# Optimization experiments

Hardware: AMD Instinct MI355X
Metric: run time of the kernel (lower is better)

## Reference

```python
import jax, jax.numpy as jnp
import numpy as np

H = 12       # num attention heads
D = 64       # head dim
K = 6        # heads activated: max(1, int(H * top_k_percent)), top_k_percent=0.5
EPS = 1e-12  # BERT LayerNorm eps


def setup_inputs() -> dict:
    key = jax.random.key(0)
    ks = jax.random.split(key, 8)
    hid = H * D
    sc = 0.02
    return {
        'hidden_states': jax.random.normal(ks[0], (8, 1024, hid), jnp.float32),
        'Wq': jax.random.normal(ks[1], (hid, hid), jnp.float32) * sc,
        'bq': jnp.zeros((hid,), jnp.float32),
        'Wk': jax.random.normal(ks[2], (hid, hid), jnp.float32) * sc,
        'bk': jnp.zeros((hid,), jnp.float32),
        'Wv': jax.random.normal(ks[3], (hid, hid), jnp.float32) * sc,
        'bv': jnp.zeros((hid,), jnp.float32),
        'Wr': jax.random.normal(ks[4], (hid, H), jnp.float32) * sc,
        'br': jnp.zeros((H,), jnp.float32),
        'Wo': jax.random.normal(ks[5], (hid, hid), jnp.float32) * sc,
        'bo': jnp.zeros((hid,), jnp.float32),
        'ln_g': jnp.ones((hid,), jnp.float32),
        'ln_b': jnp.zeros((hid,), jnp.float32),
    }


def reference(hidden_states, Wq, bq, Wk, bk, Wv, bv, Wr, br, Wo, bo, ln_g, ln_b):
    B, S, hid = hidden_states.shape
    # Router: mean-pooled tokens -> per-head logits -> straight-through top-k mask
    router_in = hidden_states.mean(axis=1)                      # [B, hid]
    logits = router_in @ Wr + br                                # [B, H]
    _, top_idx = jax.lax.top_k(logits, K)                       # [B, K]
    hard = jax.nn.one_hot(top_idx, H, dtype=logits.dtype).sum(axis=1)  # [B, H]
    head_mask = hard + logits - jax.lax.stop_gradient(logits)   # straight-through
    m = head_mask[:, :, None, None]                             # [B, H, 1, 1]

    def proj(W, b):
        return (hidden_states @ W + b).reshape(B, S, H, D).transpose(0, 2, 1, 3)

    q = proj(Wq, bq) * m
    k = proj(Wk, bk) * m
    v = proj(Wv, bv) * m

    scores = jnp.einsum('bhqd,bhkd->bhqk', q, k) / jnp.sqrt(jnp.float32(D))
    probs = jax.nn.softmax(scores, axis=-1)
    ctx = jnp.einsum('bhqk,bhkd->bhqd', probs, v)               # [B, H, S, D]
    ctx = ctx.transpose(0, 2, 1, 3).reshape(B, S, hid)

    # BertSelfOutput: dense -> (dropout=identity in eval) -> residual -> LayerNorm
    x = ctx @ Wo + bo + hidden_states
    mu = x.mean(axis=-1, keepdims=True)
    var = ((x - mu) ** 2).mean(axis=-1, keepdims=True)
    return ((x - mu) / jnp.sqrt(var + EPS)) * ln_g + ln_b
```

## Files before the change

kernel.cpp:

```cpp
#include <hip/hip_runtime.h>

typedef __bf16 bf16;
typedef __bf16 bf16x2_t __attribute__((ext_vector_type(2)));
typedef __bf16 bf16x4_t __attribute__((ext_vector_type(4)));
typedef __bf16 bf16x8 __attribute__((ext_vector_type(8)));
typedef float  f32x4  __attribute__((ext_vector_type(4)));

__device__ __forceinline__ void async16(const void* g, void* l) {
  __builtin_amdgcn_global_load_lds(
      (__attribute__((address_space(1))) void*)(g),
      (__attribute__((address_space(3))) void*)(l), 16, 0, 0);
}

__device__ __forceinline__ f32x4 mfma16(bf16x8 a, bf16x8 b, f32x4 c) {
  return __builtin_amdgcn_mfma_f32_16x16x32_bf16(a, b, c, 0, 0, 0);
}

__global__ __launch_bounds__(256) void prep_k(
    const float* __restrict__ hs, bf16* __restrict__ hsb, float* __restrict__ partial,
    const float* __restrict__ s0, const float* __restrict__ s1,
    const float* __restrict__ s2, const float* __restrict__ s3,
    bf16* __restrict__ d0, bf16* __restrict__ d1,
    bf16* __restrict__ d2, bf16* __restrict__ d3) {
  __shared__ bf16 tile[32][33];
  int id = blockIdx.x;
  int t = threadIdx.x;
  if (id < 2304) {
    int z = id / 576, rem = id % 576;
    int by = rem / 24, bx = rem % 24;
    const float* in = (z == 0) ? s0 : (z == 1) ? s1 : (z == 2) ? s2 : s3;
    bf16* out       = (z == 0) ? d0 : (z == 1) ? d1 : (z == 2) ? d2 : d3;
    int c0 = bx * 32, r0 = by * 32;
#pragma unroll
    for (int i = 0; i < 4; ++i) {
      int idx = t + i * 256;
      int r = idx >> 5, c = idx & 31;
      tile[r][c] = (bf16)in[(size_t)(r0 + r) * 768 + (c0 + c)];
    }
    __syncthreads();
#pragma unroll
    for (int i = 0; i < 4; ++i) {
      int idx = t + i * 256;
      int r = idx >> 5, c = idx & 31;
      out[(size_t)(c0 + r) * 768 + (r0 + c)] = tile[c][r];
    }
  } else {
    int id2 = id - 2304;
    int b = id2 & 7, g = id2 >> 3;
    if (t >= 192) return;
    const float* p = hs  + ((size_t)b * 1024 + g * 32) * 768 + t * 4;
    bf16*        q = hsb + ((size_t)b * 1024 + g * 32) * 768 + t * 4;
    float4 a = {0.f, 0.f, 0.f, 0.f};
    for (int s = 0; s < 32; ++s) {
      float4 v = *(const float4*)(p + (size_t)s * 768);
      a.x += v.x; a.y += v.y; a.z += v.z; a.w += v.w;
      bf16x4_t o;
      o[0] = (bf16)v.x; o[1] = (bf16)v.y; o[2] = (bf16)v.z; o[3] = (bf16)v.w;
      *(bf16x4_t*)(q + (size_t)s * 768) = o;
    }
    *(float4*)(partial + ((size_t)b * 32 + g) * 768 + t * 4) = a;
  }
}

__global__ __launch_bounds__(256) void router_final_k(const float* __restrict__ Wr,
                                                      const float* __restrict__ br,
                                                      const float* __restrict__ partial,
                                                      float* __restrict__ mask,
                                                      int* __restrict__ actH) {
  int b = blockIdx.x, t = threadIdx.x;
  int w = t >> 6;
  __shared__ float mean_s[768];
  __shared__ float red[4][12];
  __shared__ float lg[12];
  for (int c = t; c < 768; c += 256) {
    float a = 0.f;
    for (int g = 0; g < 32; ++g) a += partial[((size_t)b * 32 + g) * 768 + c];
    mean_s[c] = a * (1.0f / 1024.0f);
  }
  __syncthreads();
  float a[12];
#pragma unroll
  for (int h = 0; h < 12; ++h) a[h] = 0.f;
#pragma unroll
  for (int j = 0; j < 3; ++j) {
    int c = t + j * 256;
    float m = mean_s[c];
    const float* wr = Wr + c * 12;
#pragma unroll
    for (int h = 0; h < 12; ++h) a[h] += m * wr[h];
  }
#pragma unroll
  for (int off = 1; off < 64; off <<= 1)
#pragma unroll
    for (int h = 0; h < 12; ++h) a[h] += __shfl_xor(a[h], off);
  if ((t & 63) == 0)
#pragma unroll
    for (int h = 0; h < 12; ++h) red[w][h] = a[h];
  __syncthreads();
  if (t == 0) {
#pragma unroll
    for (int h = 0; h < 12; ++h)
      lg[h] = br[h] + red[0][h] + red[1][h] + red[2][h] + red[3][h];
    unsigned chosen = 0;
    for (int j = 0; j < 6; ++j) {
      int bi = -1; float bv = -1e30f;
      for (int h = 0; h < 12; ++h)
        if (!((chosen >> h) & 1) && lg[h] > bv) { bv = lg[h]; bi = h; }
      chosen |= 1u << bi;
    }
    int k = 0;
    for (int h = 0; h < 12; ++h) {
      mask[b * 12 + h] = ((chosen >> h) & 1) ? 1.f : 0.f;
      if ((chosen >> h) & 1) actH[b * 6 + (k++)] = h;
    }
  }
}

__global__ __launch_bounds__(256, 3) void gemm_qkv_k(
    const bf16* __restrict__ X, const bf16* __restrict__ Wcat,
    const float* __restrict__ bq, const float* __restrict__ bk, const float* __restrict__ bv,
    const int* __restrict__ actH,
    bf16* __restrict__ Qo, bf16* __restrict__ Ko, bf16* __restrict__ Vto) {
  __shared__ __align__(16) bf16 Al[128 * 64];
  __shared__ __align__(16) bf16 Bl[128 * 64];
  int mt64 = blockIdx.x;
  int sp   = blockIdx.y;
  int z    = blockIdx.z;
  int b    = mt64 >> 3;
  int h0   = actH[b * 6 + sp * 2];
  int h1   = actH[b * 6 + sp * 2 + 1];
  int m0   = mt64 * 128;

  const float* bia = (z == 0) ? bq : (z == 1) ? bk : bv;
  int t = threadIdx.x, w = t >> 6, lane = t & 63, lrow = lane & 15, quad = lane >> 4;
  int wm = (w >> 1) * 64, wn = (w & 1) * 64;

  int srow = t >> 3;
  int sch  = (t & 7) ^ (srow & 7);
  const bf16* aptr[4];
  const bf16* bptr[4];
#pragma unroll
  for (int i = 0; i < 4; ++i) {
    aptr[i] = X + (size_t)(m0 + i * 32 + srow) * 768 + sch * 8;
    int hh = (i < 2) ? h0 : h1;
    int rr = (i & 1) * 32 + srow;
    bptr[i] = Wcat + (size_t)(z * 768 + hh * 64 + rr) * 768 + sch * 8;
  }

  int ra_base = wm + lrow, rb_base = wn + lrow;
  const bf16* baA[2];
  const bf16* baB[2];
#pragma unroll
  for (int ks = 0; ks < 2; ++ks) {
    baA[ks] = &Al[ra_base * 64 + (((ks * 4 + quad) ^ (ra_base & 7)) * 8)];
    baB[ks] = &Bl[rb_base * 64 + (((ks * 4 + quad) ^ (rb_base & 7)) * 8)];
  }

  f32x4 acc[4][4];
#pragma unroll
  for (int a = 0; a < 4; ++a)
#pragma unroll
    for (int c = 0; c < 4; ++c) acc[a][c] = (f32x4){0.f, 0.f, 0.f, 0.f};

  for (int k0 = 0; k0 < 768; k0 += 64) {
#pragma unroll
    for (int i = 0; i < 4; ++i) {
      async16(aptr[i], &Al[(i * 256 + t) * 8]);
      aptr[i] += 64;
    }
#pragma unroll
    for (int i = 0; i < 4; ++i) {
      async16(bptr[i], &Bl[(i * 256 + t) * 8]);
      bptr[i] += 64;
    }
    __syncthreads();
    bf16x8 af[2][4], bfr[2][4];
#pragma unroll
    for (int ks = 0; ks < 2; ++ks)
#pragma unroll
      for (int i = 0; i < 4; ++i) {
        af[ks][i]  = *(const bf16x8*)(baA[ks] + i * 1024);
        bfr[ks][i] = *(const bf16x8*)(baB[ks] + i * 1024);
      }
#pragma unroll
    for (int ks = 0; ks < 2; ++ks)
#pragma unroll
      for (int mt = 0; mt < 4; ++mt)
#pragma unroll
        for (int nt2 = 0; nt2 < 4; ++nt2)
          acc[mt][nt2] = mfma16(af[ks][mt], bfr[ks][nt2], acc[mt][nt2]);
    __syncthreads();
  }

  float biasv[4];
#pragma unroll
  for (int nt2 = 0; nt2 < 4; ++nt2) {
    int nl = wn + nt2 * 16 + lrow;
    int hh = (nl >> 6) ? h1 : h0;
    biasv[nt2] = bia[hh * 64 + (nl & 63)];
  }

  if (z == 2) {
#pragma unroll
    for (int mt = 0; mt < 4; ++mt)
#pragma unroll
      for (int nt2 = 0; nt2 < 4; ++nt2) {
        int s = (m0 + wm + mt * 16 + quad * 4) & 1023;
        int nl = wn + nt2 * 16 + lrow;
        int hh = (nl >> 6) ? h1 : h0;
        int d = nl & 63;
        bf16x4_t pk;
#pragma unroll
        for (int r = 0; r < 4; ++r) pk[r] = (bf16)(acc[mt][nt2][r] + biasv[nt2]);
        *(bf16x4_t*)&Vto[(((size_t)b * 12 + hh) * 64 + d) * 1024 + s] = pk;
      }
  } else {
    bf16* Out = (z == 0) ? Qo : Ko;
#pragma unroll
    for (int mt = 0; mt < 4; ++mt)
#pragma unroll
      for (int nt2 = 0; nt2 < 4; ++nt2)
#pragma unroll
        for (int r = 0; r < 4; ++r) {
          int s = (m0 + wm + mt * 16 + quad * 4 + r) & 1023;
          int nl = wn + nt2 * 16 + lrow;
          int hh = (nl >> 6) ? h1 : h0;
          int d = nl & 63;
          Out[(((size_t)b * 12 + hh) * 1024 + s) * 64 + d] =
              (bf16)(acc[mt][nt2][r] + biasv[nt2]);
        }
  }
}

__global__ __launch_bounds__(256, 3) void attn_k(
    const bf16* __restrict__ Q, const bf16* __restrict__ K, const bf16* __restrict__ Vt,
    const int* __restrict__ actH, bf16* __restrict__ ctx) {
  int ai = blockIdx.x, qt = blockIdx.y;
  int bb = ai / 6, slot = ai - bb * 6;
  int h = actH[bb * 6 + slot];
  int bh = bb * 12 + h;
  int t = threadIdx.x, w = t >> 6, lane = t & 63, lrow = lane & 15, quad = lane >> 4;

  __shared__ __align__(16) bf16 K_lds[128 * 64];
  __shared__ __align__(16) bf16 V_lds[64 * 128];
  __shared__ __align__(16) bf16 P_lds[4][16 * 136];

  const bf16* Qh = Q  + (size_t)bh * 65536;
  const bf16* Kh = K  + (size_t)bh * 65536;
  const bf16* Vh = Vt + (size_t)bh * 65536;

  bf16x8 qf[2][2];
#pragma unroll
  for (int mt = 0; mt < 2; ++mt)
#pragma unroll
    for (int ks = 0; ks < 2; ++ks)
      qf[mt][ks] = *(const bf16x8*)&Qh[(size_t)(qt * 128 + w * 32 + mt * 16 + lrow) * 64 + ks * 32 + quad * 8];

  f32x4 o_acc[2][4];
  float m_i[2][4], l_i[2][4];
#pragma unroll
  for (int mt = 0; mt < 2; ++mt) {
#pragma unroll
    for (int dt = 0; dt < 4; ++dt) o_acc[mt][dt] = (f32x4){0.f, 0.f, 0.f, 0.f};
#pragma unroll
    for (int r = 0; r < 4; ++r) { m_i[mt][r] = -INFINITY; l_i[mt][r] = 0.f; }
  }

  for (int kt = 0; kt < 8; ++kt) {
#pragma unroll
    for (int i = 0; i < 4; ++i) {
      int c = i * 256 + t;
      int r = c >> 3, ch = (c & 7) ^ (r & 7);
      async16(Kh + (size_t)kt * 8192 + r * 64 + ch * 8, &K_lds[c * 8]);
    }
#pragma unroll
    for (int i = 0; i < 4; ++i) {
      int c = i * 256 + t;
      int r = c >> 4, ch = (c & 15) ^ (r & 7);
      async16(Vh + (size_t)r * 1024 + kt * 128 + ch * 8, &V_lds[c * 8]);
    }
    __syncthreads();

#pragma unroll
    for (int mt = 0; mt < 2; ++mt) {
      f32x4 s_acc[8];
#pragma unroll
      for (int nt = 0; nt < 8; ++nt) s_acc[nt] = (f32x4){0.f, 0.f, 0.f, 0.f};
      __builtin_amdgcn_s_setprio(1);
#pragma unroll
      for (int nt = 0; nt < 8; ++nt) {
        int rb = nt * 16 + lrow;
#pragma unroll
        for (int ks = 0; ks < 2; ++ks) {
          bf16x8 kf = *(const bf16x8*)&K_lds[rb * 64 + (((ks * 4 + quad) ^ (rb & 7)) * 8)];
          s_acc[nt] = mfma16(qf[mt][ks], kf, s_acc[nt]);
        }
      }
      __builtin_amdgcn_s_setprio(0);
#pragma unroll
      for (int nt = 0; nt < 8; ++nt) s_acc[nt] = s_acc[nt] * 0.125f;

      float mx[4];
#pragma unroll
      for (int r = 0; r < 4; ++r) {
        float m = s_acc[0][r];
#pragma unroll
        for (int nt = 1; nt < 8; ++nt) m = fmaxf(m, s_acc[nt][r]);
        m = fmaxf(m, __shfl_xor(m, 1));
        m = fmaxf(m, __shfl_xor(m, 2));
        m = fmaxf(m, __shfl_xor(m, 4));
        m = fmaxf(m, __shfl_xor(m, 8));
        mx[r] = m;
      }
      bool grow = false;
#pragma unroll
      for (int r = 0; r < 4; ++r) grow = grow || (mx[r] > m_i[mt][r] + 8.f);
      if (__any(grow)) {
#pragma unroll
        for (int r = 0; r < 4; ++r) {
          float mold = m_i[mt][r];
          float mnew = fmaxf(mold, mx[r]);
          float alpha = __expf(mold - mnew);
          m_i[mt][r] = mnew;
          l_i[mt][r] *= alpha;
#pragma unroll
          for (int dt = 0; dt < 4; ++dt) o_acc[mt][dt][r] *= alpha;
        }
      }
#pragma unroll
      for (int r = 0; r < 4; ++r) {
        float mnew = m_i[mt][r];
        float rs = 0.f;
#pragma unroll
        for (int nt = 0; nt < 8; ++nt) {
          float pv = __expf(s_acc[nt][r] - mnew);
          rs += pv;
          P_lds[w][(quad * 4 + r) * 136 + nt * 16 + lrow] = (bf16)pv;
        }
        rs += __shfl_xor(rs, 1);
        rs += __shfl_xor(rs, 2);
        rs += __shfl_xor(rs, 4);
        rs += __shfl_xor(rs, 8);
        l_i[mt][r] += rs;
      }

      bf16x8 pf[4];
#pragma unroll
      for (int ks = 0; ks < 4; ++ks)
        pf[ks] = *(const bf16x8*)&P_lds[w][lrow * 136 + ks * 32 + quad * 8];
      __builtin_amdgcn_s_setprio(1);
#pragma unroll
      for (int dt = 0; dt < 4; ++dt) {
        int rv = dt * 16 + lrow;
#pragma unroll
        for (int ks = 0; ks < 4; ++ks) {
          bf16x8 vf = *(const bf16x8*)&V_lds[rv * 128 + (((ks * 4 + quad) ^ (rv & 7)) * 8)];
          o_acc[mt][dt] = mfma16(pf[ks], vf, o_acc[mt][dt]);
        }
      }
      __builtin_amdgcn_s_setprio(0);
    }
    __syncthreads();
  }

#pragma unroll
  for (int mt = 0; mt < 2; ++mt)
#pragma unroll
    for (int r = 0; r < 4; ++r) {
      float inv = 1.0f / l_i[mt][r];
      int s = qt * 128 + w * 32 + mt * 16 + quad * 4 + r;
#pragma unroll
      for (int dt = 0; dt < 4; ++dt) {
        int d = dt * 16 + lrow;
        ctx[((size_t)(bb * 1024 + s)) * 768 + h * 64 + d] = (bf16)(o_acc[mt][dt][r] * inv);
      }
    }
}

__global__ __launch_bounds__(256, 3) void gemm_out_k(
    const bf16* __restrict__ Cx, const bf16* __restrict__ Wot,
    const float* __restrict__ bo, const float* __restrict__ res,
    const float* __restrict__ mask,
    float* __restrict__ xo) {
  __shared__ __align__(16) bf16 Al[128 * 64];
  __shared__ __align__(16) bf16 Bl[128 * 64];
  int bid = blockIdx.x;
  int xcd = bid & 7, idx = bid >> 3;
  int nt = idx % 6, mt8 = idx / 6;
  int m0 = (mt8 * 8 + xcd) * 128;
  int n0 = nt * 128;
  int t = threadIdx.x, w = t >> 6, lane = t & 63, lrow = lane & 15, quad = lane >> 4;
  int wm = (w >> 1) * 64, wn = (w & 1) * 64;

  int bb = m0 >> 10;
  unsigned am = 0;
#pragma unroll
  for (int hh = 0; hh < 12; ++hh)
    am |= (mask[bb * 12 + hh] != 0.f) ? (1u << hh) : 0u;

  int srow = t >> 3;
  int sch  = (t & 7) ^ (srow & 7);
  const bf16* aptr[4];
  const bf16* bptr[4];
#pragma unroll
  for (int i = 0; i < 4; ++i) {
    aptr[i] = Cx  + (size_t)(m0 + i * 32 + srow) * 768 + sch * 8;
    bptr[i] = Wot + (size_t)(n0 + i * 32 + srow) * 768 + sch * 8;
  }
  int ra_base = wm + lrow, rb_base = wn + lrow;
  const bf16* baA[2];
  const bf16* baB[2];
#pragma unroll
  for (int ks = 0; ks < 2; ++ks) {
    baA[ks] = &Al[ra_base * 64 + (((ks * 4 + quad) ^ (ra_base & 7)) * 8)];
    baB[ks] = &Bl[rb_base * 64 + (((ks * 4 + quad) ^ (rb_base & 7)) * 8)];
  }

  f32x4 acc[4][4];
#pragma unroll
  for (int a = 0; a < 4; ++a)
#pragma unroll
    for (int b = 0; b < 4; ++b) acc[a][b] = (f32x4){0.f, 0.f, 0.f, 0.f};

  for (int k0 = 0; k0 < 768; k0 += 64) {
    if (am & (1u << (k0 >> 6))) {
#pragma unroll
      for (int i = 0; i < 4; ++i) async16(aptr[i], &Al[(i * 256 + t) * 8]);
#pragma unroll
      for (int i = 0; i < 4; ++i) async16(bptr[i], &Bl[(i * 256 + t) * 8]);
      __syncthreads();
      bf16x8 af[2][4], bfr[2][4];
#pragma unroll
      for (int ks = 0; ks < 2; ++ks)
#pragma unroll
        for (int i = 0; i < 4; ++i) {
          af[ks][i]  = *(const bf16x8*)(baA[ks] + i * 1024);
          bfr[ks][i] = *(const bf16x8*)(baB[ks] + i * 1024);
        }
#pragma unroll
      for (int ks = 0; ks < 2; ++ks)
#pragma unroll
        for (int mt = 0; mt < 4; ++mt)
#pragma unroll
          for (int nt2 = 0; nt2 < 4; ++nt2)
            acc[mt][nt2] = mfma16(af[ks][mt], bfr[ks][nt2], acc[mt][nt2]);
      __syncthreads();
    }
#pragma unroll
    for (int i = 0; i < 4; ++i) { aptr[i] += 64; bptr[i] += 64; }
  }

  float biasv[4];
#pragma unroll
  for (int nt2 = 0; nt2 < 4; ++nt2) biasv[nt2] = bo[n0 + wn + nt2 * 16 + lrow];

#pragma unroll
  for (int mt = 0; mt < 4; ++mt)
#pragma unroll
    for (int nt2 = 0; nt2 < 4; ++nt2)
#pragma unroll
      for (int r = 0; r < 4; ++r) {
        int m = m0 + wm + mt * 16 + quad * 4 + r;
        int n = n0 + wn + nt2 * 16 + lrow;
        xo[(size_t)m * 768 + n] = acc[mt][nt2][r] + biasv[nt2] + res[(size_t)m * 768 + n];
      }
}

__global__ __launch_bounds__(256) void ln_k(const float* __restrict__ x,
                                            const float* __restrict__ g,
                                            const float* __restrict__ be,
                                            float* __restrict__ out) {
  int t = threadIdx.x, w = t >> 6, lane = t & 63;
  int row = blockIdx.x * 4 + w;
  const float4* xr4 = (const float4*)(x + (size_t)row * 768);
  float4 v0 = xr4[lane], v1 = xr4[lane + 64], v2 = xr4[lane + 128];
  float s  = v0.x + v0.y + v0.z + v0.w + v1.x + v1.y + v1.z + v1.w
           + v2.x + v2.y + v2.z + v2.w;
  float s2 = v0.x*v0.x + v0.y*v0.y + v0.z*v0.z + v0.w*v0.w
           + v1.x*v1.x + v1.y*v1.y + v1.z*v1.z + v1.w*v1.w
           + v2.x*v2.x + v2.y*v2.y + v2.z*v2.z + v2.w*v2.w;
#pragma unroll
  for (int off = 32; off > 0; off >>= 1) {
    s  += __shfl_xor(s, off);
    s2 += __shfl_xor(s2, off);
  }
  float mu = s * (1.0f / 768.0f);
  float var = s2 * (1.0f / 768.0f) - mu * mu;
  float rsq = rsqrtf(var + 1e-12f);
  const float4* g4 = (const float4*)g;
  const float4* b4 = (const float4*)be;
  float4* or4 = (float4*)(out + (size_t)row * 768);
  float4 gv, bv, o;
  gv = g4[lane];       bv = b4[lane];
  o.x = (v0.x - mu) * rsq * gv.x + bv.x; o.y = (v0.y - mu) * rsq * gv.y + bv.y;
  o.z = (v0.z - mu) * rsq * gv.z + bv.z; o.w = (v0.w - mu) * rsq * gv.w + bv.w;
  or4[lane] = o;
  gv = g4[lane + 64];  bv = b4[lane + 64];
  o.x = (v1.x - mu) * rsq * gv.x + bv.x; o.y = (v1.y - mu) * rsq * gv.y + bv.y;
  o.z = (v1.z - mu) * rsq * gv.z + bv.z; o.w = (v1.w - mu) * rsq * gv.w + bv.w;
  or4[lane + 64] = o;
  gv = g4[lane + 128]; bv = b4[lane + 128];
  o.x = (v2.x - mu) * rsq * gv.x + bv.x; o.y = (v2.y - mu) * rsq * gv.y + bv.y;
  o.z = (v2.z - mu) * rsq * gv.z + bv.z; o.w = (v2.w - mu) * rsq * gv.w + bv.w;
  or4[lane + 128] = o;
}

extern "C" void kernel_launch(void* const* d_in, const int* in_sizes, int n_in,
                              void* d_out, int out_size, void* d_ws, size_t ws_size,
                              hipStream_t stream) {
  const float* hs  = (const float*)d_in[0];
  const float* Wq  = (const float*)d_in[1];
  const float* bq  = (const float*)d_in[2];
  const float* Wk  = (const float*)d_in[3];
  const float* bk  = (const float*)d_in[4];
  const float* Wv  = (const float*)d_in[5];
  const float* bv  = (const float*)d_in[6];
  const float* Wr  = (const float*)d_in[7];
  const float* br  = (const float*)d_in[8];
  const float* Wo  = (const float*)d_in[9];
  const float* bo  = (const float*)d_in[10];
  const float* lng = (const float*)d_in[11];
  const float* lnb = (const float*)d_in[12];
  float* out = (float*)d_out;
  dim3 blk(256);

  char* p = (char*)d_ws;
  float* maskp = (float*)p; p += 512;
  int*   actI  = (int*)p;   p += 256;
  float* partial = (float*)p; p += (size_t)8 * 32 * 768 * 4;
  bf16* hsb  = (bf16*)p; p += (size_t)8192 * 768 * 2;
  bf16* Wcat = (bf16*)p; p += (size_t)2304 * 768 * 2;
  bf16* Wot  = (bf16*)p; p += (size_t)768 * 768 * 2;

  prep_k<<<dim3(2560), blk, 0, stream>>>(hs, hsb, partial,
      Wq, Wk, Wv, Wo, Wcat, Wcat + 768 * 768, Wcat + 1536 * 768, Wot);
  router_final_k<<<dim3(8), blk, 0, stream>>>(Wr, br, partial, maskp, actI);

  size_t used_common = (size_t)(p - (char*)d_ws);
  size_t need_big = used_common + 3 * (size_t)8192 * 768 * 2;

  if (ws_size >= need_big) {
    char* qk_base = p;
    bf16* Qb  = (bf16*)p; p += (size_t)8192 * 768 * 2;
    bf16* Kb  = (bf16*)p; p += (size_t)8192 * 768 * 2;
    bf16* Vtb = (bf16*)p;
    float* Xb = (float*)qk_base;
    bf16* Ctx = (bf16*)d_out;

    gemm_qkv_k<<<dim3(64, 3, 3), blk, 0, stream>>>(hsb, Wcat, bq, bk, bv, actI, Qb, Kb, Vtb);
    attn_k<<<dim3(48, 8), blk, 0, stream>>>(Qb, Kb, Vtb, actI, Ctx);
    gemm_out_k<<<dim3(8 * 8 * 6), blk, 0, stream>>>(Ctx, Wot, bo, hs, maskp, Xb);
    ln_k<<<dim3(2048), blk, 0, stream>>>(Xb, lng, lnb, out);
  } else {
    bf16* Qb  = (bf16*)p; p += (size_t)1024 * 768 * 2;
    bf16* Kb  = (bf16*)p; p += (size_t)1024 * 768 * 2;
    bf16* Vtb = (bf16*)p; p += (size_t)1024 * 768 * 2;
    bf16* Ctx = (bf16*)p; p += (size_t)1024 * 768 * 2;
    float* Xb = (float*)p; p += (size_t)1024 * 768 * 4;

    for (int b = 0; b < 8; ++b) {
      const bf16* hsb_b = hsb + (size_t)b * 1024 * 768;
      const float* hs_b = hs + (size_t)b * 1024 * 768;
      float* outb = out + (size_t)b * 1024 * 768;
      gemm_qkv_k<<<dim3(8, 3, 3), blk, 0, stream>>>(hsb_b, Wcat, bq, bk, bv, actI + b * 6, Qb, Kb, Vtb);
      attn_k<<<dim3(6, 8), blk, 0, stream>>>(Qb, Kb, Vtb, actI + b * 6, Ctx);
      gemm_out_k<<<dim3(8 * 1 * 6), blk, 0, stream>>>(Ctx, Wot, bo, hs_b, maskp + b * 12, Xb);
      ln_k<<<dim3(256), blk, 0, stream>>>(Xb, lng, lnb, outb);
    }
  }
}
```

Before: 210.8 us.

## Split attention over two key halves with a flash-decoding style combine kernel

The attention kernel now splits the 1024-key sequence into two halves along a new grid z dimension, doubling the block count from 384 to 768 so the GPU's compute units are better filled. Each half writes unnormalised bf16 partial outputs plus per-row max and sum, and a new combine kernel merges them with log-sum-exp rescaling into the context buffer. This adds an extra launch, a round trip of partial results through memory, and bf16 rounding of the unnormalised partials. The context buffer is also moved into the hsb region.

```diff
diff --git a/kernel.cpp b/kernel.cpp
--- a/kernel.cpp
+++ b/kernel.cpp
@@ -234,8 +234,10 @@
 
 __global__ __launch_bounds__(256, 3) void attn_k(
     const bf16* __restrict__ Q, const bf16* __restrict__ K, const bf16* __restrict__ Vt,
-    const int* __restrict__ actH, bf16* __restrict__ ctx) {
-  int ai = blockIdx.x, qt = blockIdx.y;
+    const int* __restrict__ actH,
+    bf16* __restrict__ opart, float* __restrict__ mpart, float* __restrict__ lpart,
+    int nbh) {
+  int ai = blockIdx.x, qt = blockIdx.y, z = blockIdx.z;
   int bb = ai / 6, slot = ai - bb * 6;
   int h = actH[bb * 6 + slot];
   int bh = bb * 12 + h;
@@ -246,8 +248,9 @@
   __shared__ __align__(16) bf16 P_lds[4][16 * 136];
 
   const bf16* Qh = Q  + (size_t)bh * 65536;
-  const bf16* Kh = K  + (size_t)bh * 65536;
+  const bf16* Kh = K  + (size_t)bh * 65536 + (size_t)z * 32768;
   const bf16* Vh = Vt + (size_t)bh * 65536;
+  int vcol0 = z * 512;
 
   bf16x8 qf[2][2];
 #pragma unroll
@@ -266,7 +269,7 @@
     for (int r = 0; r < 4; ++r) { m_i[mt][r] = -INFINITY; l_i[mt][r] = 0.f; }
   }
 
-  for (int kt = 0; kt < 8; ++kt) {
+  for (int kt = 0; kt < 4; ++kt) {
 #pragma unroll
     for (int i = 0; i < 4; ++i) {
       int c = i * 256 + t;
@@ -277,7 +280,7 @@
     for (int i = 0; i < 4; ++i) {
       int c = i * 256 + t;
       int r = c >> 4, ch = (c & 15) ^ (r & 7);
-      async16(Vh + (size_t)r * 1024 + kt * 128 + ch * 8, &V_lds[c * 8]);
+      async16(Vh + (size_t)r * 1024 + vcol0 + kt * 128 + ch * 8, &V_lds[c * 8]);
     }
     __syncthreads();
 
@@ -363,18 +366,45 @@
     __syncthreads();
   }
 
+  size_t tile = ((size_t)(z * nbh + ai) * 8 + qt);
 #pragma unroll
   for (int mt = 0; mt < 2; ++mt)
 #pragma unroll
     for (int r = 0; r < 4; ++r) {
-      float inv = 1.0f / l_i[mt][r];
-      int s = qt * 128 + w * 32 + mt * 16 + quad * 4 + r;
-#pragma unroll
-      for (int dt = 0; dt < 4; ++dt) {
-        int d = dt * 16 + lrow;
-        ctx[((size_t)(bb * 1024 + s)) * 768 + h * 64 + d] = (bf16)(o_acc[mt][dt][r] * inv);
-      }
-    }
+      int srow = w * 32 + mt * 16 + quad * 4 + r;
+      if (lrow == 0) {
+        mpart[tile * 128 + srow] = m_i[mt][r];
+        lpart[tile * 128 + srow] = l_i[mt][r];
+      }
+#pragma unroll
+      for (int dt = 0; dt < 4; ++dt)
+        opart[(tile * 128 + srow) * 64 + dt * 16 + lrow] = (bf16)o_acc[mt][dt][r];
+    }
+}
+
+__global__ __launch_bounds__(256) void combine_k(
+    const bf16* __restrict__ opart, const float* __restrict__ mpart,
+    const float* __restrict__ lpart, const int* __restrict__ actH,
+    bf16* __restrict__ ctx, int nbh) {
+  int ai = blockIdx.x, qt = blockIdx.y;
+  int bb = ai / 6, slot = ai - bb * 6;
+  int h = actH[bb * 6 + slot];
+  int t = threadIdx.x, w = t >> 6, lane = t & 63;
+  size_t t1 = ((size_t)ai * 8 + qt) * 128;
+  size_t t2 = ((size_t)(nbh + ai) * 8 + qt) * 128;
+  for (int i = 0; i < 32; ++i) {
+    int row = w * 32 + i;
+    float m1 = mpart[t1 + row], l1 = lpart[t1 + row];
+    float m2 = mpart[t2 + row], l2 = lpart[t2 + row];
+    float M = fmaxf(m1, m2);
+    float a1 = __expf(m1 - M), a2 = __expf(m2 - M);
+    float inv = 1.0f / (l1 * a1 + l2 * a2);
+    float o1 = (float)opart[(t1 + row) * 64 + lane];
+    float o2 = (float)opart[(t2 + row) * 64 + lane];
+    int s = qt * 128 + row;
+    ctx[((size_t)(bb * 1024 + s)) * 768 + h * 64 + lane] =
+        (bf16)((o1 * a1 + o2 * a2) * inv);
+  }
 }
 
 __global__ __launch_bounds__(256, 3) void gemm_out_k(
@@ -545,10 +575,14 @@
     bf16* Kb  = (bf16*)p; p += (size_t)8192 * 768 * 2;
     bf16* Vtb = (bf16*)p;
     float* Xb = (float*)qk_base;
-    bf16* Ctx = (bf16*)d_out;
+    bf16* Ctx = hsb;
+    bf16*  opart = (bf16*)d_out;
+    float* mpart = (float*)((char*)d_out + (size_t)13 * 1024 * 1024);
+    float* lpart = mpart + 2 * 48 * 8 * 128;
 
     gemm_qkv_k<<<dim3(64, 3, 3), blk, 0, stream>>>(hsb, Wcat, bq, bk, bv, actI, Qb, Kb, Vtb);
-    attn_k<<<dim3(48, 8), blk, 0, stream>>>(Qb, Kb, Vtb, actI, Ctx);
+    attn_k<<<dim3(48, 8, 2), blk, 0, stream>>>(Qb, Kb, Vtb, actI, opart, mpart, lpart, 48);
+    combine_k<<<dim3(48, 8), blk, 0, stream>>>(opart, mpart, lpart, actI, Ctx, 48);
     gemm_out_k<<<dim3(8 * 8 * 6), blk, 0, stream>>>(Ctx, Wot, bo, hs, maskp, Xb);
     ln_k<<<dim3(2048), blk, 0, stream>>>(Xb, lng, lnb, out);
   } else {
@@ -557,13 +591,17 @@
     bf16* Vtb = (bf16*)p; p += (size_t)1024 * 768 * 2;
     bf16* Ctx = (bf16*)p; p += (size_t)1024 * 768 * 2;
     float* Xb = (float*)p; p += (size_t)1024 * 768 * 4;
+    bf16*  opart = (bf16*)p; p += (size_t)2 * 6 * 8 * 128 * 64 * 2;
+    float* mpart = (float*)p; p += (size_t)2 * 6 * 8 * 128 * 4;
+    float* lpart = (float*)p; p += (size_t)2 * 6 * 8 * 128 * 4;
 
     for (int b = 0; b < 8; ++b) {
       const bf16* hsb_b = hsb + (size_t)b * 1024 * 768;
       const float* hs_b = hs + (size_t)b * 1024 * 768;
       float* outb = out + (size_t)b * 1024 * 768;
       gemm_qkv_k<<<dim3(8, 3, 3), blk, 0, stream>>>(hsb_b, Wcat, bq, bk, bv, actI + b * 6, Qb, Kb, Vtb);
-      attn_k<<<dim3(6, 8), blk, 0, stream>>>(Qb, Kb, Vtb, actI + b * 6, Ctx);
+      attn_k<<<dim3(6, 8, 2), blk, 0, stream>>>(Qb, Kb, Vtb, actI + b * 6, opart, mpart, lpart, 6);
+      combine_k<<<dim3(6, 8), blk, 0, stream>>>(opart, mpart, lpart, actI + b * 6, Ctx, 6);
       gemm_out_k<<<dim3(8 * 1 * 6), blk, 0, stream>>>(Ctx, Wot, bo, hs_b, maskp + b * 12, Xb);
       ln_k<<<dim3(256), blk, 0, stream>>>(Xb, lng, lnb, outb);
     }
```

Measured after the change: 207.8 us. Within noise of the previous version (-1.4%).
